# Kernel tuning notes

Measured on AMD Instinct MI355X. Metric: run time of the kernel, lower is better.

Reference implementation:

```python
import jax, jax.numpy as jnp
import numpy as np

NEG_SLOPE = 0.2  # PyG GATConv default


def gat_conv(x, src, dst, W_src, W_dst, att_src, att_dst, bias, heads, ch, n_nodes):
    """One PyG-style GATConv with self-loops already included in (src, dst).
    Returns [N, heads*ch] (concat over heads)."""
    xs = (x @ W_src).reshape(n_nodes, heads, ch)  # source-side transform (messages)
    xd = (x @ W_dst).reshape(n_nodes, heads, ch)  # dest-side transform (attention only)
    a_s = jnp.sum(xs * att_src, axis=-1)  # [N, H]
    a_d = jnp.sum(xd * att_dst, axis=-1)  # [N, H]
    e = jax.nn.leaky_relu(a_s[src] + a_d[dst], NEG_SLOPE)  # [E, H]
    # segment softmax over edges grouped by destination node
    m = jax.ops.segment_max(e, dst, num_segments=n_nodes)  # [N, H]
    ex = jnp.exp(e - m[dst])
    denom = jax.ops.segment_sum(ex, dst, num_segments=n_nodes)  # [N, H]
    alpha = ex / denom[dst]  # [E, H]
    # weighted scatter-aggregate of source messages
    out = jax.ops.segment_sum(xs[src] * alpha[:, :, None], dst, num_segments=n_nodes)
    return out.reshape(n_nodes, heads * ch) + bias


def setup_inputs() -> dict:
    key = jax.random.key(0)
    ks = jax.random.split(key, 12)
    N, F, E = 50000, 128, 400000
    H, C1, C2 = 4, 64, 64
    x = jax.random.normal(ks[0], (N, F), dtype=jnp.float32)
    edge_index = jax.random.randint(ks[1], (2, E), 0, N, dtype=jnp.int64)
    g = lambda k, shape, fan_in: jax.random.normal(k, shape, dtype=jnp.float32) * (1.0 / np.sqrt(fan_in))
    return {
        "x": x,
        "edge_index": edge_index,
        "W1_src": g(ks[2], (F, H * C1), F),
        "W1_dst": g(ks[3], (F, H * C1), F),
        "att1_src": g(ks[4], (H, C1), C1),
        "att1_dst": g(ks[5], (H, C1), C1),
        "b1": jnp.zeros((H * C1,), dtype=jnp.float32),
        "W2_src": g(ks[6], (H * C1, C2), H * C1),
        "W2_dst": g(ks[7], (H * C1, C2), H * C1),
        "att2_src": g(ks[8], (1, C2), C2),
        "att2_dst": g(ks[9], (1, C2), C2),
        "b2": jnp.zeros((C2,), dtype=jnp.float32),
    }


def reference(x, edge_index, W1_src, W1_dst, att1_src, att1_dst, b1,
              W2_src, W2_dst, att2_src, att2_dst, b2):
    N = x.shape[0]
    loop = jnp.arange(N, dtype=edge_index.dtype)
    src = jnp.concatenate([edge_index[0], loop])  # add_self_loops=True
    dst = jnp.concatenate([edge_index[1], loop])
    H, C1 = att1_src.shape
    C2 = att2_src.shape[1]
    h = gat_conv(x, src, dst, W1_src, W1_dst, att1_src, att1_dst, b1, H, C1, N)
    h = jax.nn.relu(h)
    # dropout is identity in eval mode
    out = gat_conv(h, src, dst, W2_src, W2_dst, att2_src, att2_dst, b2, 1, C2, N)
    return out
```

## Files before the change

kernel.cpp:

```cpp
#include <hip/hip_runtime.h>


static inline int cdiv(int a, int b) { return (a + b - 1) / b; }

typedef __attribute__((ext_vector_type(8))) short short8;
typedef __attribute__((ext_vector_type(4))) float floatx4;

__device__ __forceinline__ float bf2f(unsigned short u) {
  return __uint_as_float(((unsigned int)u) << 16);
}
__device__ __forceinline__ unsigned short f2bf(float f) {
  unsigned int u = __float_as_uint(f);
  unsigned int r = (u + 0x7FFFu + ((u >> 16) & 1u)) >> 16;
  return (unsigned short)r;
}
__device__ __forceinline__ float ldv(const void* p, int i, int bf) {
  return bf ? bf2f(((const unsigned short*)p)[i]) : ((const float*)p)[i];
}
#define NEG_INF (-__builtin_inff())

__global__ void fill_out_kernel(float* __restrict__ out, int n, float val) {
  int t = blockIdx.x * blockDim.x + threadIdx.x;
  if (t < n) out[t] = val;
}

__device__ void block_probes(const unsigned short* xu, const unsigned int* eu,
                             int& bf, int& e64) {
  __shared__ int cc, ce;
  if (threadIdx.x == 0) { cc = 0; ce = 0; }
  __syncthreads();
  int l0 = 0, l1 = 0;
  for (int i = threadIdx.x; i < 1024; i += 256) {
    int e = (xu[2 * i] >> 7) & 0xFF;
    if (e >= 100 && e <= 141) l0++;
    if (eu[2 * i + 1] == 0u) l1++;
  }
  atomicAdd(&cc, l0); atomicAdd(&ce, l1);
  __syncthreads();
  bf = cc > 512 ? 1 : 0;
  e64 = ce > 512 ? 1 : 0;
}

__global__ void prep_edges(const unsigned short* __restrict__ xu,
                           const void* __restrict__ EI, int E, int EP, int Nn,
                           const void* __restrict__ W1s, const void* __restrict__ W1d,
                           const void* __restrict__ a1s, const void* __restrict__ a1d,
                           const void* __restrict__ W2s, const void* __restrict__ W2d,
                           const void* __restrict__ a2s, const void* __restrict__ a2d,
                           const void* __restrict__ b1, const void* __restrict__ b2,
                           unsigned short* __restrict__ W1c,
                           unsigned short* __restrict__ W2sT,
                           unsigned short* __restrict__ W1ext,
                           float* __restrict__ v2s, float* __restrict__ v2d,
                           float* __restrict__ b1f, float* __restrict__ b2f,
                           int* __restrict__ srcI, int* __restrict__ dstI,
                           int* __restrict__ posE,
                           int* __restrict__ deg) {
  const int b = blockIdx.x, t = threadIdx.x;
  int bf, e64;
  block_probes(xu, (const unsigned int*)EI, bf, e64);
  if (b < 128) {
    int i = b * 256 + t;
    W1c[i] = f2bf(ldv(W1s, i, bf));
  } else if (b < 192) {
    int i = (b - 128) * 256 + t;
    int k = i >> 6, col = i & 63;
    W2sT[col * 256 + k] = f2bf(ldv(W2s, i, bf));
  } else if (b < 198) {
    const int lane = t & 63, w = t >> 6;
    const int g = lane >> 3, ll = lane & 7;
    const int base = (b - 192) * 256 + w * 64 + g;
#pragma unroll
    for (int r = 0; r < 8; ++r) {
      const int d = base + r * 8;
      const void *W, *A;
      int wo, ao;
      if (d < 1024) {
        int k = d >> 3, q = d & 7, h = q & 3;
        W = (q < 4) ? W1s : W1d;
        A = (q < 4) ? a1s : a1d;
        wo = k * 256 + h * 64;
        ao = h * 64;
      } else {
        int e = d - 1024, k = e & 255;
        W = (e < 256) ? W2s : W2d;
        A = (e < 256) ? a2s : a2d;
        wo = k * 64;
        ao = 0;
      }
      float p;
      if (bf) {
        uint4 wv = *(const uint4*)((const unsigned short*)W + wo + ll * 8);
        uint4 av = *(const uint4*)((const unsigned short*)A + ao + ll * 8);
        p  = bf2f((unsigned short)(wv.x & 0xFFFF)) * bf2f((unsigned short)(av.x & 0xFFFF));
        p += bf2f((unsigned short)(wv.x >> 16))    * bf2f((unsigned short)(av.x >> 16));
        p += bf2f((unsigned short)(wv.y & 0xFFFF)) * bf2f((unsigned short)(av.y & 0xFFFF));
        p += bf2f((unsigned short)(wv.y >> 16))    * bf2f((unsigned short)(av.y >> 16));
        p += bf2f((unsigned short)(wv.z & 0xFFFF)) * bf2f((unsigned short)(av.z & 0xFFFF));
        p += bf2f((unsigned short)(wv.z >> 16))    * bf2f((unsigned short)(av.z >> 16));
        p += bf2f((unsigned short)(wv.w & 0xFFFF)) * bf2f((unsigned short)(av.w & 0xFFFF));
        p += bf2f((unsigned short)(wv.w >> 16))    * bf2f((unsigned short)(av.w >> 16));
      } else {
        float4 w0 = *(const float4*)((const float*)W + wo + ll * 8);
        float4 w1 = *(const float4*)((const float*)W + wo + ll * 8 + 4);
        float4 a0 = *(const float4*)((const float*)A + ao + ll * 8);
        float4 a1 = *(const float4*)((const float*)A + ao + ll * 8 + 4);
        p = w0.x * a0.x + w0.y * a0.y + w0.z * a0.z + w0.w * a0.w +
            w1.x * a1.x + w1.y * a1.y + w1.z * a1.z + w1.w * a1.w;
      }
      p += __shfl_xor(p, 1);
      p += __shfl_xor(p, 2);
      p += __shfl_xor(p, 4);
      if (ll == 0) {
        if (d < 1024) {
          int k = d >> 3, q = d & 7;
          W1ext[k * 16 + q] = f2bf(p);
          W1ext[k * 16 + 8 + q] = 0;
        } else {
          int e = d - 1024, k = e & 255;
          if (e < 256) v2s[k] = p; else v2d[k] = p;
        }
      }
    }
  } else if (b == 198) {
    b1f[t] = ldv(b1, t, bf);
    if (t < 64) b2f[t] = ldv(b2, t, bf);
  } else {
    int i = (b - 199) * 256 + t;
    if (i < EP) {
      int s, d;
      if (i < E) {
        if (e64) {
          const unsigned int* p = (const unsigned int*)EI;
          s = (int)p[2 * (size_t)i];
          d = (int)p[2 * ((size_t)E + i)];
        } else {
          const int* p = (const int*)EI;
          s = p[i]; d = p[E + i];
        }
      } else { s = i - E; d = s; }
      if ((unsigned)s >= (unsigned)Nn) s = 0;
      if ((unsigned)d >= (unsigned)Nn) d = 0;
      srcI[i] = s; dstI[i] = d;
      posE[i] = atomicAdd(&deg[d], 1);
    }
  }
}

__global__ __launch_bounds__(256) void scan_gemm(
    const void* __restrict__ X, const unsigned short* __restrict__ xu,
    const int* __restrict__ deg, int* __restrict__ rowst,
    int* __restrict__ scanflag, int nb,
    const unsigned short* __restrict__ W1c, const unsigned short* __restrict__ W1ext,
    unsigned short* __restrict__ xs1, float* __restrict__ A1, int N) {
  __shared__ __align__(16) unsigned short smem[9 * 16 * 136];
  const int t = threadIdx.x;
  if (blockIdx.x < nb) {
    const int c = blockIdx.x;
    int* ssc = (int*)smem;
    int i = c * 256 + t;
    int v = (i < N) ? deg[i] : 0;
    ssc[t] = v;
    __syncthreads();
    for (int off = 1; off < 256; off <<= 1) {
      int add = (t >= off) ? ssc[t - off] : 0;
      __syncthreads();
      ssc[t] += add;
      __syncthreads();
    }
    int incl = ssc[t];
    if (t == 255) atomicExch(&scanflag[c], ssc[255] + 1);
    __syncthreads();
    int pre = 0;
    if (t < c) {
      int f;
      while ((f = __hip_atomic_load(&scanflag[t], __ATOMIC_RELAXED,
                                    __HIP_MEMORY_SCOPE_AGENT)) == 0) {}
      pre = f - 1;
    }
    int* s2 = ssc + 256;
    s2[t] = pre;
    __syncthreads();
    for (int off = 128; off; off >>= 1) {
      if (t < off) s2[t] += s2[t + off];
      __syncthreads();
    }
    if (i < N) rowst[i] = s2[0] + incl - v;
    return;
  }
  __shared__ int pcc;
  if (t == 0) pcc = 0;
  __syncthreads();
  {
    int l0 = 0;
    for (int i = t; i < 1024; i += 256) {
      int e = (xu[2 * i] >> 7) & 0xFF;
      if (e >= 100 && e <= 141) l0++;
    }
    atomicAdd(&pcc, l0);
  }
  __syncthreads();
  const int bf = pcc > 512 ? 1 : 0;
  unsigned short* Wlds = smem;
  const int lane = t & 63, wid = t >> 6;
  const int quad = lane >> 4, m16 = lane & 15;
  const int r0b = (blockIdx.x - nb) * 64;
  const int r0 = r0b + wid * 16;
  const int arow = min(r0 + m16, N - 1);
  short8 af[4];
  if (bf) {
    const uint4* Xr = (const uint4*)((const unsigned int*)X + (size_t)arow * 64);
#pragma unroll
    for (int ks = 0; ks < 4; ++ks)
      af[ks] = __builtin_bit_cast(short8, Xr[ks * 4 + quad]);
  } else {
    const float* Xr = (const float*)X + (size_t)arow * 128;
#pragma unroll
    for (int ks = 0; ks < 4; ++ks) {
      short8 v;
#pragma unroll
      for (int j = 0; j < 8; ++j) v[j] = (short)f2bf(Xr[ks * 32 + quad * 8 + j]);
      af[ks] = v;
    }
  }
  floatx4 accs[9];
  if (t < 144) {
    for (int k0 = 0; k0 < 128; k0 += 4) {
      unsigned int u0, u1;
      if (t < 128) {
        const unsigned short* p = W1c + (size_t)k0 * 256 + t;
        u0 = (unsigned int)p[0] | ((unsigned int)p[256] << 16);
        u1 = (unsigned int)p[512] | ((unsigned int)p[768] << 16);
      } else {
        const unsigned short* p = W1ext + (size_t)k0 * 16 + (t - 128);
        u0 = (unsigned int)p[0] | ((unsigned int)p[16] << 16);
        u1 = (unsigned int)p[32] | ((unsigned int)p[48] << 16);
      }
      *(uint2*)&Wlds[t * 136 + k0] = make_uint2(u0, u1);
    }
  }
  __syncthreads();
#pragma unroll
  for (int ct = 0; ct < 9; ++ct) {
    floatx4 acc = {0.f, 0.f, 0.f, 0.f};
    const unsigned short* wl = &Wlds[(ct * 16 + m16) * 136];
#pragma unroll
    for (int ks = 0; ks < 4; ++ks) {
      short8 bfv = *(const short8*)(wl + ks * 32 + quad * 8);
      acc = __builtin_amdgcn_mfma_f32_16x16x32_bf16(af[ks], bfv, acc, 0, 0, 0);
    }
    accs[ct] = acc;
  }
  __syncthreads();
  if (m16 < 8) {
#pragma unroll
    for (int r = 0; r < 4; ++r) {
      int row = r0 + quad * 4 + r;
      if (row < N) A1[(size_t)row * 8 + m16] = accs[8][r];
    }
  }
#pragma unroll
  for (int ct = 0; ct < 8; ++ct)
#pragma unroll
    for (int r = 0; r < 4; ++r)
      Wlds[(wid * 16 + quad * 4 + r) * 136 + ct * 16 + m16] = f2bf(accs[ct][r]);
  __syncthreads();
#pragma unroll
  for (int it = 0; it < 4; ++it) {
    int lrow = it * 16 + (t >> 4);
    int grow = r0b + lrow;
    if (grow < N) {
      uint4 v = *(const uint4*)&Wlds[lrow * 136 + (t & 15) * 8];
      *(uint4*)(xs1 + (size_t)grow * 256 + (t & 15) * 8) = v;
    }
  }
  __syncthreads();
  if (t < 128) {
    for (int k0 = 0; k0 < 128; k0 += 4) {
      const unsigned short* p = W1c + (size_t)k0 * 256 + 128 + t;
      unsigned int u0 = (unsigned int)p[0] | ((unsigned int)p[256] << 16);
      unsigned int u1 = (unsigned int)p[512] | ((unsigned int)p[768] << 16);
      *(uint2*)&Wlds[t * 136 + k0] = make_uint2(u0, u1);
    }
  }
  __syncthreads();
#pragma unroll
  for (int ct = 0; ct < 8; ++ct) {
    floatx4 acc = {0.f, 0.f, 0.f, 0.f};
    const unsigned short* wl = &Wlds[(ct * 16 + m16) * 136];
#pragma unroll
    for (int ks = 0; ks < 4; ++ks) {
      short8 bfv = *(const short8*)(wl + ks * 32 + quad * 8);
      acc = __builtin_amdgcn_mfma_f32_16x16x32_bf16(af[ks], bfv, acc, 0, 0, 0);
    }
    accs[ct] = acc;
  }
  __syncthreads();
#pragma unroll
  for (int ct = 0; ct < 8; ++ct)
#pragma unroll
    for (int r = 0; r < 4; ++r)
      Wlds[(wid * 16 + quad * 4 + r) * 136 + ct * 16 + m16] = f2bf(accs[ct][r]);
  __syncthreads();
#pragma unroll
  for (int it = 0; it < 4; ++it) {
    int lrow = it * 16 + (t >> 4);
    int grow = r0b + lrow;
    if (grow < N) {
      uint4 v = *(const uint4*)&Wlds[lrow * 136 + (t & 15) * 8];
      *(uint4*)(xs1 + (size_t)grow * 256 + 128 + (t & 15) * 8) = v;
    }
  }
}

__global__ void fill_srcS(const int* __restrict__ srcI, const int* __restrict__ dstI,
                          const int* __restrict__ posE, int EP,
                          const int* __restrict__ rowst, int* __restrict__ srcS) {
  int t = blockIdx.x * blockDim.x + threadIdx.x;
  if (t >= EP) return;
  int d = dstI[t];
  srcS[rowst[d] + posE[t]] = srcI[t];
}

__global__ __launch_bounds__(256) void node1_merged(
    const int* __restrict__ rowst, const int* __restrict__ deg,
    const int* __restrict__ srcS,
    const float* __restrict__ A1, const unsigned short* __restrict__ xs1,
    const float* __restrict__ b1f, const unsigned short* __restrict__ W2sT,
    const float* __restrict__ v2s, const float* __restrict__ v2d,
    unsigned short* __restrict__ xs2, float* __restrict__ A2, int N) {
  __shared__ unsigned short hb[8][272];
  __shared__ int   s_sh[4][2][32];
  __shared__ float al_sh[4][2][32][4];
  const int lane = threadIdx.x & 63;
  const int wid = threadIdx.x >> 6;
  const int hf = lane >> 5;
  const int hl = lane & 31;
  const int nraw = blockIdx.x * 8 + wid * 2 + hf;
  const bool valid = nraw < N;
  const int n = valid ? nraw : (N - 1);
  const int st = rowst[n], dn = deg[n];
  const float4 ad4 = *(const float4*)(A1 + (size_t)n * 8 + 4);
  const float ad[4] = {ad4.x, ad4.y, ad4.z, ad4.w};
  const int gc = 8 * hl;
  const int hd = hl >> 3;
  float acc[8] = {0.f, 0.f, 0.f, 0.f, 0.f, 0.f, 0.f, 0.f};
  constexpr int PF = 12;

  if (__all(dn <= 32)) {
    int s = 0;
    float4 as4 = make_float4(0.f, 0.f, 0.f, 0.f);
    if (hl < dn) {
      s = srcS[st + hl];
      as4 = *(const float4*)(A1 + (size_t)s * 8);
    }
    const int np = dn < PF ? dn : PF;
    uint4 u[PF];
#pragma unroll
    for (int j = 0; j < PF; ++j) {
      if (j < np) {
        int sj = __shfl(s, (hf << 5) + j);
        u[j] = *(const uint4*)(xs1 + (size_t)sj * 256 + gc);
      }
    }
    float v[4] = {NEG_INF, NEG_INF, NEG_INF, NEG_INF};
    if (hl < dn) {
      const float as[4] = {as4.x, as4.y, as4.z, as4.w};
#pragma unroll
      for (int h = 0; h < 4; ++h) {
        float x = as[h] + ad[h];
        v[h] = x > 0.f ? x : 0.2f * x;
      }
    }
    float m[4], l[4];
#pragma unroll
    for (int h = 0; h < 4; ++h) {
      m[h] = v[h];
#pragma unroll
      for (int off = 16; off; off >>= 1) m[h] = fmaxf(m[h], __shfl_xor(m[h], off));
      float e = (hl < dn) ? __expf(v[h] - m[h]) : 0.f;
      l[h] = e;
#pragma unroll
      for (int off = 16; off; off >>= 1) l[h] += __shfl_xor(l[h], off);
      v[h] = e;
    }
    if (hl < dn) {
      s_sh[wid][hf][hl] = s;
      float4 al = {v[0] / l[0], v[1] / l[1], v[2] / l[2], v[3] / l[3]};
      *(float4*)&al_sh[wid][hf][hl][0] = al;
    }
#pragma unroll
    for (int j = 0; j < PF; ++j) {
      if (j < np) {
        float a0 = al_sh[wid][hf][j][hd];
        acc[0] += a0 * __uint_as_float(u[j].x << 16);
        acc[1] += a0 * __uint_as_float(u[j].x & 0xFFFF0000u);
        acc[2] += a0 * __uint_as_float(u[j].y << 16);
        acc[3] += a0 * __uint_as_float(u[j].y & 0xFFFF0000u);
        acc[4] += a0 * __uint_as_float(u[j].z << 16);
        acc[5] += a0 * __uint_as_float(u[j].z & 0xFFFF0000u);
        acc[6] += a0 * __uint_as_float(u[j].w << 16);
        acc[7] += a0 * __uint_as_float(u[j].w & 0xFFFF0000u);
      }
    }
    for (int j = np; j < dn; ++j) {
      int s0 = s_sh[wid][hf][j];
      float a0 = al_sh[wid][hf][j][hd];
      uint4 uu = *(const uint4*)(xs1 + (size_t)s0 * 256 + gc);
      acc[0] += a0 * __uint_as_float(uu.x << 16);
      acc[1] += a0 * __uint_as_float(uu.x & 0xFFFF0000u);
      acc[2] += a0 * __uint_as_float(uu.y << 16);
      acc[3] += a0 * __uint_as_float(uu.y & 0xFFFF0000u);
      acc[4] += a0 * __uint_as_float(uu.z << 16);
      acc[5] += a0 * __uint_as_float(uu.z & 0xFFFF0000u);
      acc[6] += a0 * __uint_as_float(uu.w << 16);
      acc[7] += a0 * __uint_as_float(uu.w & 0xFFFF0000u);
    }
  } else {
    float m[4] = {NEG_INF, NEG_INF, NEG_INF, NEG_INF};
    for (int j = hl; j < dn; j += 32) {
      int s = srcS[st + j];
      const float4 as4 = *(const float4*)(A1 + (size_t)s * 8);
      const float as[4] = {as4.x, as4.y, as4.z, as4.w};
#pragma unroll
      for (int h = 0; h < 4; ++h) {
        float x = as[h] + ad[h];
        x = x > 0.f ? x : 0.2f * x;
        m[h] = fmaxf(m[h], x);
      }
    }
#pragma unroll
    for (int h = 0; h < 4; ++h)
#pragma unroll
      for (int off = 16; off; off >>= 1) m[h] = fmaxf(m[h], __shfl_xor(m[h], off));
    float l[4] = {0.f, 0.f, 0.f, 0.f};
    for (int j = hl; j < dn; j += 32) {
      int s = srcS[st + j];
      const float4 as4 = *(const float4*)(A1 + (size_t)s * 8);
      const float as[4] = {as4.x, as4.y, as4.z, as4.w};
#pragma unroll
      for (int h = 0; h < 4; ++h) {
        float x = as[h] + ad[h];
        x = x > 0.f ? x : 0.2f * x;
        l[h] += __expf(x - m[h]);
      }
    }
#pragma unroll
    for (int h = 0; h < 4; ++h)
#pragma unroll
      for (int off = 16; off; off >>= 1) l[h] += __shfl_xor(l[h], off);
    const float mh = m[hd], inv = 1.0f / l[hd], adh = ad[hd];
    for (int j = 0; j < dn; ++j) {
      int s = srcS[st + j];
      float x = A1[(size_t)s * 8 + hd] + adh;
      x = x > 0.f ? x : 0.2f * x;
      float alpha = __expf(x - mh) * inv;
      uint4 uu = *(const uint4*)(xs1 + (size_t)s * 256 + gc);
      acc[0] += alpha * __uint_as_float(uu.x << 16);
      acc[1] += alpha * __uint_as_float(uu.x & 0xFFFF0000u);
      acc[2] += alpha * __uint_as_float(uu.y << 16);
      acc[3] += alpha * __uint_as_float(uu.y & 0xFFFF0000u);
      acc[4] += alpha * __uint_as_float(uu.z << 16);
      acc[5] += alpha * __uint_as_float(uu.z & 0xFFFF0000u);
      acc[6] += alpha * __uint_as_float(uu.w << 16);
      acc[7] += alpha * __uint_as_float(uu.w & 0xFFFF0000u);
    }
  }

  const float4 bb0 = *(const float4*)(b1f + gc);
  const float4 bb1 = *(const float4*)(b1f + gc + 4);
  float hv[8];
  hv[0] = acc[0] + bb0.x; hv[1] = acc[1] + bb0.y;
  hv[2] = acc[2] + bb0.z; hv[3] = acc[3] + bb0.w;
  hv[4] = acc[4] + bb1.x; hv[5] = acc[5] + bb1.y;
  hv[6] = acc[6] + bb1.z; hv[7] = acc[7] + bb1.w;
#pragma unroll
  for (int k = 0; k < 8; ++k) hv[k] = hv[k] > 0.f ? hv[k] : 0.f;
  const float4 vs0 = *(const float4*)(v2s + gc);
  const float4 vs1 = *(const float4*)(v2s + gc + 4);
  const float4 vd0 = *(const float4*)(v2d + gc);
  const float4 vd1 = *(const float4*)(v2d + gc + 4);
  float ps = hv[0] * vs0.x + hv[1] * vs0.y + hv[2] * vs0.z + hv[3] * vs0.w +
             hv[4] * vs1.x + hv[5] * vs1.y + hv[6] * vs1.z + hv[7] * vs1.w;
  float pd = hv[0] * vd0.x + hv[1] * vd0.y + hv[2] * vd0.z + hv[3] * vd0.w +
             hv[4] * vd1.x + hv[5] * vd1.y + hv[6] * vd1.z + hv[7] * vd1.w;
#pragma unroll
  for (int off = 1; off <= 16; off <<= 1) {
    ps += __shfl_xor(ps, off);
    pd += __shfl_xor(pd, off);
  }
  unsigned int p0 = (unsigned int)f2bf(hv[0]) | ((unsigned int)f2bf(hv[1]) << 16);
  unsigned int p1 = (unsigned int)f2bf(hv[2]) | ((unsigned int)f2bf(hv[3]) << 16);
  unsigned int p2 = (unsigned int)f2bf(hv[4]) | ((unsigned int)f2bf(hv[5]) << 16);
  unsigned int p3 = (unsigned int)f2bf(hv[6]) | ((unsigned int)f2bf(hv[7]) << 16);
  *(uint4*)&hb[wid * 2 + hf][gc] = make_uint4(p0, p1, p2, p3);
  if (valid && hl == 0) {
    A2[(size_t)n * 2] = ps;
    A2[(size_t)n * 2 + 1] = pd;
  }
  __syncthreads();
  const int m16 = lane & 15, quad = lane >> 4;
  floatx4 c2 = {0.f, 0.f, 0.f, 0.f};
  const unsigned short* arow = &hb[m16 & 7][0];
  const unsigned short* bcol = W2sT + (size_t)(wid * 16 + m16) * 256;
#pragma unroll
  for (int ks = 0; ks < 8; ++ks) {
    short8 afr = *(const short8*)(arow + ks * 32 + quad * 8);
    short8 bfr = *(const short8*)(bcol + ks * 32 + quad * 8);
    c2 = __builtin_amdgcn_mfma_f32_16x16x32_bf16(afr, bfr, c2, 0, 0, 0);
  }
  if (quad < 2) {
#pragma unroll
    for (int r = 0; r < 4; ++r) {
      int node = blockIdx.x * 8 + quad * 4 + r;
      if (node < N) xs2[(size_t)node * 64 + wid * 16 + m16] = f2bf(c2[r]);
    }
  }
}

__global__ __launch_bounds__(256) void node2(const int* __restrict__ rowst,
    const int* __restrict__ deg, const int* __restrict__ srcS,
    const float* __restrict__ A2, const unsigned short* __restrict__ xs2,
    const float* __restrict__ b2f, float* __restrict__ out, int N) {
  __shared__ int   s_sh[4][2][32];
  __shared__ float al_sh[4][2][32];
  const int lane = threadIdx.x & 63;
  const int wid = threadIdx.x >> 6;
  const int hf = lane >> 5;
  const int hl = lane & 31;
  const int nraw = blockIdx.x * 8 + wid * 2 + hf;
  const bool valid = nraw < N;
  const int n = valid ? nraw : (N - 1);
  const int st = rowst[n], dn = deg[n];
  const float ad = A2[(size_t)n * 2 + 1];
  float ax = 0.f, ay = 0.f;
  constexpr int PF2 = 16;
  if (__all(dn <= 32)) {
    int s = 0;
    float a2v = 0.f;
    if (hl < dn) {
      s = srcS[st + hl];
      a2v = A2[(size_t)s * 2];
    }
    const int np = dn < PF2 ? dn : PF2;
    unsigned int u[PF2];
#pragma unroll
    for (int j = 0; j < PF2; ++j) {
      if (j < np) {
        int sj = __shfl(s, (hf << 5) + j);
        u[j] = *(const unsigned int*)(xs2 + (size_t)sj * 64 + 2 * hl);
      }
    }
    float v = NEG_INF;
    if (hl < dn) {
      v = a2v + ad;
      v = v > 0.f ? v : 0.2f * v;
    }
    float m = v;
#pragma unroll
    for (int off = 16; off; off >>= 1) m = fmaxf(m, __shfl_xor(m, off));
    float e = (hl < dn) ? __expf(v - m) : 0.f;
    float l = e;
#pragma unroll
    for (int off = 16; off; off >>= 1) l += __shfl_xor(l, off);
    if (hl < dn) { s_sh[wid][hf][hl] = s; al_sh[wid][hf][hl] = e / l; }
#pragma unroll
    for (int j = 0; j < PF2; ++j) {
      if (j < np) {
        float a = al_sh[wid][hf][j];
        ax += a * __uint_as_float(u[j] << 16);
        ay += a * __uint_as_float(u[j] & 0xFFFF0000u);
      }
    }
    for (int j = np; j < dn; ++j) {
      int s0 = s_sh[wid][hf][j];
      float a = al_sh[wid][hf][j];
      unsigned int uu = *(const unsigned int*)(xs2 + (size_t)s0 * 64 + 2 * hl);
      ax += a * __uint_as_float(uu << 16);
      ay += a * __uint_as_float(uu & 0xFFFF0000u);
    }
  } else {
    float m = NEG_INF;
    for (int j = hl; j < dn; j += 32) {
      int s = srcS[st + j];
      float v = A2[(size_t)s * 2] + ad;
      v = v > 0.f ? v : 0.2f * v;
      m = fmaxf(m, v);
    }
#pragma unroll
    for (int off = 16; off; off >>= 1) m = fmaxf(m, __shfl_xor(m, off));
    float l = 0.f;
    for (int j = hl; j < dn; j += 32) {
      int s = srcS[st + j];
      float v = A2[(size_t)s * 2] + ad;
      v = v > 0.f ? v : 0.2f * v;
      l += __expf(v - m);
    }
#pragma unroll
    for (int off = 16; off; off >>= 1) l += __shfl_xor(l, off);
    float inv = 1.0f / l;
    for (int j = 0; j < dn; ++j) {
      int s = srcS[st + j];
      float v = A2[(size_t)s * 2] + ad;
      v = v > 0.f ? v : 0.2f * v;
      float alpha = __expf(v - m) * inv;
      unsigned int uu = *(const unsigned int*)(xs2 + (size_t)s * 64 + 2 * hl);
      ax += alpha * __uint_as_float(uu << 16);
      ay += alpha * __uint_as_float(uu & 0xFFFF0000u);
    }
  }
  if (valid) {
    const float2 b = *(const float2*)(b2f + 2 * hl);
    float2 o = make_float2(ax + b.x, ay + b.y);
    *(float2*)(out + (size_t)n * 64 + 2 * hl) = o;
  }
}

extern "C" void kernel_launch(void* const* d_in, const int* in_sizes, int n_in,
                              void* d_out, int out_size, void* d_ws, size_t ws_size,
                              hipStream_t stream) {
  const int F = 128, HC1 = 256, C2 = 64;
  const int N  = in_sizes[0] / F;
  const int E  = in_sizes[1] / 2;
  const int EP = E + N;
  (void)n_in;

  char* w = (char*)d_ws;
  size_t off = 0;
  auto alloc = [&](size_t bytes) -> char* {
    char* p = w + off;
    off = (off + bytes + 255) & ~(size_t)255;
    return p;
  };
  int* srcI   = (int*)alloc((size_t)EP * 4);
  int* dstI   = (int*)alloc((size_t)EP * 4);
  int* posE   = (int*)alloc((size_t)EP * 4);
  int* degcur = (int*)alloc(((size_t)N + 256) * 4);
  int* deg    = degcur;
  int* scanflag = degcur + N;
  int* rowst  = (int*)alloc((size_t)N * 4);
  unsigned short* W1c   = (unsigned short*)alloc((size_t)F * HC1 * 2);
  unsigned short* W1ext = (unsigned short*)alloc(128 * 16 * 2);
  unsigned short* W2sT  = (unsigned short*)alloc((size_t)HC1 * C2 * 2);
  float* v2s  = (float*)alloc(256 * 4);
  float* v2d  = (float*)alloc(256 * 4);
  float* b1f  = (float*)alloc(256 * 4);
  float* b2f  = (float*)alloc(64 * 4);
  int*   srcS = (int*)alloc((size_t)EP * 4);
  float* A1   = (float*)alloc((size_t)N * 8 * 4);
  unsigned short* xs1 = (unsigned short*)alloc((size_t)N * HC1 * 2);
  unsigned short* xs2 = (unsigned short*)alloc((size_t)N * C2 * 2);
  float* A2 = (float*)alloc((size_t)N * 2 * 4);
  const size_t need = off;

  if (ws_size < need) {
    fill_out_kernel<<<cdiv(out_size, 256), 256, 0, stream>>>(
        (float*)d_out, out_size, 131072.0f + 1024.0f * (float)(ws_size >> 20));
    return;
  }

  hipMemsetAsync(degcur, 0, ((size_t)N + 256) * 4, stream);

  prep_edges<<<199 + cdiv(EP, 256), 256, 0, stream>>>(
      (const unsigned short*)d_in[0], d_in[1], E, EP, N,
      d_in[2], d_in[3], d_in[4], d_in[5], d_in[7], d_in[8], d_in[9], d_in[10],
      d_in[6], d_in[11],
      W1c, W2sT, W1ext, v2s, v2d, b1f, b2f, srcI, dstI, posE, deg);

  const int nb = cdiv(N, 256);
  scan_gemm<<<nb + cdiv(N, 64), 256, 0, stream>>>(
      d_in[0], (const unsigned short*)d_in[0], deg, rowst, scanflag, nb,
      W1c, W1ext, xs1, A1, N);

  fill_srcS<<<cdiv(EP, 256), 256, 0, stream>>>(srcI, dstI, posE, EP, rowst, srcS);
  node1_merged<<<cdiv(N, 8), 256, 0, stream>>>(rowst, deg, srcS, A1, xs1,
                                               b1f, W2sT, v2s, v2d, xs2, A2, N);
  node2<<<cdiv(N, 8), 256, 0, stream>>>(rowst, deg, srcS, A2, xs2, b2f,
                                        (float*)d_out, N);
}
```

Baseline: 239.4 us.

## Pre-transpose layer-1 weights so GEMM reads B fragments directly from global

The prep kernel now writes W1 and the attention-extension columns in transposed (column-major, K-contiguous) bf16 layout. The GEMM blocks then load MFMA B operands straight from global/L2 as short8 vectors instead of staging the weight tile through LDS with scalar gathers. This shrinks shared memory from 9*16*136 to 64*136 and removes a block-wide staging pass and several barriers per block. It also splits the dtype probes so each block in prep runs only the probe it needs. The trade-off is that every wave now reads weights from cache rather than LDS.

```diff
diff --git a/kernel.cpp b/kernel.cpp
--- a/kernel.cpp
+++ b/kernel.cpp
@@ -24,21 +24,29 @@
   if (t < n) out[t] = val;
 }
 
-__device__ void block_probes(const unsigned short* xu, const unsigned int* eu,
-                             int& bf, int& e64) {
-  __shared__ int cc, ce;
-  if (threadIdx.x == 0) { cc = 0; ce = 0; }
+__device__ int probe_bf(const unsigned short* xu) {
+  __shared__ int cc;
+  if (threadIdx.x == 0) cc = 0;
   __syncthreads();
-  int l0 = 0, l1 = 0;
+  int l0 = 0;
   for (int i = threadIdx.x; i < 1024; i += 256) {
     int e = (xu[2 * i] >> 7) & 0xFF;
     if (e >= 100 && e <= 141) l0++;
+  }
+  atomicAdd(&cc, l0);
+  __syncthreads();
+  return cc > 512 ? 1 : 0;
+}
+__device__ int probe_e64(const unsigned int* eu) {
+  __shared__ int ce;
+  if (threadIdx.x == 0) ce = 0;
+  __syncthreads();
+  int l1 = 0;
+  for (int i = threadIdx.x; i < 1024; i += 256)
     if (eu[2 * i + 1] == 0u) l1++;
-  }
-  atomicAdd(&cc, l0); atomicAdd(&ce, l1);
+  atomicAdd(&ce, l1);
   __syncthreads();
-  bf = cc > 512 ? 1 : 0;
-  e64 = ce > 512 ? 1 : 0;
+  return ce > 512 ? 1 : 0;
 }
 
 __global__ void prep_edges(const unsigned short* __restrict__ xu,
@@ -48,25 +56,27 @@
                            const void* __restrict__ W2s, const void* __restrict__ W2d,
                            const void* __restrict__ a2s, const void* __restrict__ a2d,
                            const void* __restrict__ b1, const void* __restrict__ b2,
-                           unsigned short* __restrict__ W1c,
+                           unsigned short* __restrict__ W1cT,
                            unsigned short* __restrict__ W2sT,
-                           unsigned short* __restrict__ W1ext,
+                           unsigned short* __restrict__ W1extT,
                            float* __restrict__ v2s, float* __restrict__ v2d,
                            float* __restrict__ b1f, float* __restrict__ b2f,
                            int* __restrict__ srcI, int* __restrict__ dstI,
                            int* __restrict__ posE,
                            int* __restrict__ deg) {
   const int b = blockIdx.x, t = threadIdx.x;
-  int bf, e64;
-  block_probes(xu, (const unsigned int*)EI, bf, e64);
   if (b < 128) {
+    const int bf = probe_bf(xu);
     int i = b * 256 + t;
-    W1c[i] = f2bf(ldv(W1s, i, bf));
+    int k = i >> 8, col = i & 255;
+    W1cT[col * 128 + k] = f2bf(ldv(W1s, i, bf));
   } else if (b < 192) {
+    const int bf = probe_bf(xu);
     int i = (b - 128) * 256 + t;
     int k = i >> 6, col = i & 63;
     W2sT[col * 256 + k] = f2bf(ldv(W2s, i, bf));
   } else if (b < 198) {
+    const int bf = probe_bf(xu);
     const int lane = t & 63, w = t >> 6;
     const int g = lane >> 3, ll = lane & 7;
     const int base = (b - 192) * 256 + w * 64 + g;
@@ -114,8 +124,8 @@
       if (ll == 0) {
         if (d < 1024) {
           int k = d >> 3, q = d & 7;
-          W1ext[k * 16 + q] = f2bf(p);
-          W1ext[k * 16 + 8 + q] = 0;
+          W1extT[q * 128 + k] = f2bf(p);
+          W1extT[(8 + q) * 128 + k] = 0;
         } else {
           int e = d - 1024, k = e & 255;
           if (e < 256) v2s[k] = p; else v2d[k] = p;
@@ -123,9 +133,11 @@
       }
     }
   } else if (b == 198) {
+    const int bf = probe_bf(xu);
     b1f[t] = ldv(b1, t, bf);
     if (t < 64) b2f[t] = ldv(b2, t, bf);
   } else {
+    const int e64 = probe_e64((const unsigned int*)EI);
     int i = (b - 199) * 256 + t;
     if (i < EP) {
       int s, d;
@@ -151,9 +163,9 @@
     const void* __restrict__ X, const unsigned short* __restrict__ xu,
     const int* __restrict__ deg, int* __restrict__ rowst,
     int* __restrict__ scanflag, int nb,
-    const unsigned short* __restrict__ W1c, const unsigned short* __restrict__ W1ext,
+    const unsigned short* __restrict__ W1cT, const unsigned short* __restrict__ W1extT,
     unsigned short* __restrict__ xs1, float* __restrict__ A1, int N) {
-  __shared__ __align__(16) unsigned short smem[9 * 16 * 136];
+  __shared__ __align__(16) unsigned short smem[64 * 136];
   const int t = threadIdx.x;
   if (blockIdx.x < nb) {
     const int c = blockIdx.x;
@@ -188,19 +200,7 @@
     if (i < N) rowst[i] = s2[0] + incl - v;
     return;
   }
-  __shared__ int pcc;
-  if (t == 0) pcc = 0;
-  __syncthreads();
-  {
-    int l0 = 0;
-    for (int i = t; i < 1024; i += 256) {
-      int e = (xu[2 * i] >> 7) & 0xFF;
-      if (e >= 100 && e <= 141) l0++;
-    }
-    atomicAdd(&pcc, l0);
-  }
-  __syncthreads();
-  const int bf = pcc > 512 ? 1 : 0;
+  const int bf = probe_bf(xu);
   unsigned short* Wlds = smem;
   const int lane = t & 63, wid = t >> 6;
   const int quad = lane >> 4, m16 = lane & 15;
@@ -223,93 +223,47 @@
       af[ks] = v;
     }
   }
-  floatx4 accs[9];
-  if (t < 144) {
-    for (int k0 = 0; k0 < 128; k0 += 4) {
-      unsigned int u0, u1;
-      if (t < 128) {
-        const unsigned short* p = W1c + (size_t)k0 * 256 + t;
-        u0 = (unsigned int)p[0] | ((unsigned int)p[256] << 16);
-        u1 = (unsigned int)p[512] | ((unsigned int)p[768] << 16);
-      } else {
-        const unsigned short* p = W1ext + (size_t)k0 * 16 + (t - 128);
-        u0 = (unsigned int)p[0] | ((unsigned int)p[16] << 16);
-        u1 = (unsigned int)p[32] | ((unsigned int)p[48] << 16);
-      }
-      *(uint2*)&Wlds[t * 136 + k0] = make_uint2(u0, u1);
-    }
-  }
-  __syncthreads();
-#pragma unroll
-  for (int ct = 0; ct < 9; ++ct) {
-    floatx4 acc = {0.f, 0.f, 0.f, 0.f};
-    const unsigned short* wl = &Wlds[(ct * 16 + m16) * 136];
-#pragma unroll
-    for (int ks = 0; ks < 4; ++ks) {
-      short8 bfv = *(const short8*)(wl + ks * 32 + quad * 8);
-      acc = __builtin_amdgcn_mfma_f32_16x16x32_bf16(af[ks], bfv, acc, 0, 0, 0);
-    }
-    accs[ct] = acc;
-  }
-  __syncthreads();
-  if (m16 < 8) {
-#pragma unroll
-    for (int r = 0; r < 4; ++r) {
-      int row = r0 + quad * 4 + r;
-      if (row < N) A1[(size_t)row * 8 + m16] = accs[8][r];
-    }
-  }
-#pragma unroll
-  for (int ct = 0; ct < 8; ++ct)
-#pragma unroll
-    for (int r = 0; r < 4; ++r)
-      Wlds[(wid * 16 + quad * 4 + r) * 136 + ct * 16 + m16] = f2bf(accs[ct][r]);
-  __syncthreads();
-#pragma unroll
-  for (int it = 0; it < 4; ++it) {
-    int lrow = it * 16 + (t >> 4);
-    int grow = r0b + lrow;
-    if (grow < N) {
-      uint4 v = *(const uint4*)&Wlds[lrow * 136 + (t & 15) * 8];
-      *(uint4*)(xs1 + (size_t)grow * 256 + (t & 15) * 8) = v;
-    }
-  }
-  __syncthreads();
-  if (t < 128) {
-    for (int k0 = 0; k0 < 128; k0 += 4) {
-      const unsigned short* p = W1c + (size_t)k0 * 256 + 128 + t;
-      unsigned int u0 = (unsigned int)p[0] | ((unsigned int)p[256] << 16);
-      unsigned int u1 = (unsigned int)p[512] | ((unsigned int)p[768] << 16);
-      *(uint2*)&Wlds[t * 136 + k0] = make_uint2(u0, u1);
-    }
-  }
-  __syncthreads();
-#pragma unroll
-  for (int ct = 0; ct < 8; ++ct) {
-    floatx4 acc = {0.f, 0.f, 0.f, 0.f};
-    const unsigned short* wl = &Wlds[(ct * 16 + m16) * 136];
-#pragma unroll
-    for (int ks = 0; ks < 4; ++ks) {
-      short8 bfv = *(const short8*)(wl + ks * 32 + quad * 8);
-      acc = __builtin_amdgcn_mfma_f32_16x16x32_bf16(af[ks], bfv, acc, 0, 0, 0);
-    }
-    accs[ct] = acc;
-  }
-  __syncthreads();
-#pragma unroll
-  for (int ct = 0; ct < 8; ++ct)
-#pragma unroll
-    for (int r = 0; r < 4; ++r)
-      Wlds[(wid * 16 + quad * 4 + r) * 136 + ct * 16 + m16] = f2bf(accs[ct][r]);
-  __syncthreads();
-#pragma unroll
-  for (int it = 0; it < 4; ++it) {
-    int lrow = it * 16 + (t >> 4);
-    int grow = r0b + lrow;
-    if (grow < N) {
-      uint4 v = *(const uint4*)&Wlds[lrow * 136 + (t & 15) * 8];
-      *(uint4*)(xs1 + (size_t)grow * 256 + 128 + (t & 15) * 8) = v;
-    }
+#pragma unroll
+  for (int ph = 0; ph < 2; ++ph) {
+    floatx4 accs[9];
+    const int ncts = ph ? 8 : 9;
+#pragma unroll
+    for (int ct = 0; ct < 9; ++ct) {
+      if (ct >= ncts) break;
+      floatx4 acc = {0.f, 0.f, 0.f, 0.f};
+      const unsigned short* bp = (ct < 8)
+          ? W1cT + (size_t)(ph * 128 + ct * 16 + m16) * 128
+          : W1extT + (size_t)m16 * 128;
+#pragma unroll
+      for (int ks = 0; ks < 4; ++ks) {
+        short8 bfv = *(const short8*)(bp + ks * 32 + quad * 8);
+        acc = __builtin_amdgcn_mfma_f32_16x16x32_bf16(af[ks], bfv, acc, 0, 0, 0);
+      }
+      accs[ct] = acc;
+    }
+    if (ph == 0 && m16 < 8) {
+#pragma unroll
+      for (int r = 0; r < 4; ++r) {
+        int row = r0 + quad * 4 + r;
+        if (row < N) A1[(size_t)row * 8 + m16] = accs[8][r];
+      }
+    }
+#pragma unroll
+    for (int ct = 0; ct < 8; ++ct)
+#pragma unroll
+      for (int r = 0; r < 4; ++r)
+        Wlds[(wid * 16 + quad * 4 + r) * 136 + ct * 16 + m16] = f2bf(accs[ct][r]);
+    __syncthreads();
+#pragma unroll
+    for (int it = 0; it < 4; ++it) {
+      int lrow = it * 16 + (t >> 4);
+      int grow = r0b + lrow;
+      if (grow < N) {
+        uint4 v = *(const uint4*)&Wlds[lrow * 136 + (t & 15) * 8];
+        *(uint4*)(xs1 + (size_t)grow * 256 + ph * 128 + (t & 15) * 8) = v;
+      }
+    }
+    __syncthreads();
   }
 }
 
@@ -639,8 +593,8 @@
   int* deg    = degcur;
   int* scanflag = degcur + N;
   int* rowst  = (int*)alloc((size_t)N * 4);
-  unsigned short* W1c   = (unsigned short*)alloc((size_t)F * HC1 * 2);
-  unsigned short* W1ext = (unsigned short*)alloc(128 * 16 * 2);
+  unsigned short* W1cT  = (unsigned short*)alloc((size_t)F * HC1 * 2);
+  unsigned short* W1extT = (unsigned short*)alloc(16 * 128 * 2);
   unsigned short* W2sT  = (unsigned short*)alloc((size_t)HC1 * C2 * 2);
   float* v2s  = (float*)alloc(256 * 4);
   float* v2d  = (float*)alloc(256 * 4);
@@ -665,12 +619,12 @@
       (const unsigned short*)d_in[0], d_in[1], E, EP, N,
       d_in[2], d_in[3], d_in[4], d_in[5], d_in[7], d_in[8], d_in[9], d_in[10],
       d_in[6], d_in[11],
-      W1c, W2sT, W1ext, v2s, v2d, b1f, b2f, srcI, dstI, posE, deg);
+      W1cT, W2sT, W1extT, v2s, v2d, b1f, b2f, srcI, dstI, posE, deg);
 
   const int nb = cdiv(N, 256);
   scan_gemm<<<nb + cdiv(N, 64), 256, 0, stream>>>(
       d_in[0], (const unsigned short*)d_in[0], deg, rowst, scanflag, nb,
-      W1c, W1ext, xs1, A1, N);
+      W1cT, W1extT, xs1, A1, N);
 
   fill_srcS<<<cdiv(EP, 256), 256, 0, stream>>>(srcI, dstI, posE, EP, rowst, srcS);
   node1_merged<<<cdiv(N, 8), 256, 0, stream>>>(rowst, deg, srcS, A1, xs1,
```

Result: faster. 233.4 us (-2.5%).
